# Performance work log

Hardware: AMD Instinct MI355X
Metric: run time of the kernel (lower is better)

## Reference

```python
import jax, jax.numpy as jnp
import numpy as np

D_MODEL = 1024
PATTERNS = 8
BETA = 1.0


def setup_inputs() -> dict:
    key = jax.random.key(0)
    k_h, k_p, k_w, k_b = jax.random.split(key, 4)
    h = jax.random.normal(k_h, (8, 8192, D_MODEL), dtype=jnp.float32)
    patterns = jax.random.normal(k_p, (PATTERNS, D_MODEL), dtype=jnp.float32)
    # nn.Linear(d_model, d_model): weight [out, in], bias [out]
    bound = 1.0 / np.sqrt(D_MODEL)
    proj_w = jax.random.uniform(k_w, (D_MODEL, D_MODEL), minval=-bound, maxval=bound, dtype=jnp.float32)
    proj_b = jax.random.uniform(k_b, (D_MODEL,), minval=-bound, maxval=bound, dtype=jnp.float32)
    return {"h": h, "patterns": patterns, "proj_w": proj_w, "proj_b": proj_b}


def reference(h, patterns, proj_w, proj_b):
    # scores: [B, S, P] = softmax(beta * h @ patterns^T)
    scores = jax.nn.softmax(BETA * jnp.einsum("bsd,pd->bsp", h, patterns), axis=-1)
    # read: [B, S, D]
    read = jnp.einsum("bsp,pd->bsd", scores, patterns)
    # proj(h + read): Linear applies x @ W^T + b
    return jnp.einsum("bsd,ed->bse", h + read, proj_w) + proj_b
```

## Files before the change

### kernel.cpp

```cpp
#include <hip/hip_runtime.h>
#include <hip/hip_bf16.h>
#include <stdint.h>

#define DM 1024
#define NPAT 8
#define NKT 16
#define LDS_A 0
#define LDS_B 65536

typedef __bf16 bf16x8_t __attribute__((ext_vector_type(8)));
typedef float f32x4_t __attribute__((ext_vector_type(4)));
typedef unsigned short u16;

typedef const __attribute__((address_space(1))) void* gas_ptr;
typedef __attribute__((address_space(3))) void* las_ptr;

__device__ __forceinline__ u16 f2bf(float x) {
  uint32_t u = __float_as_uint(x);
  uint32_t r = (u + 0x7FFFu + ((u >> 16) & 1u)) >> 16;
  return (u16)r;
}

__global__ __launch_bounds__(256) void k0_cvt_w(const float* __restrict__ w,
                                                u16* __restrict__ wb) {
  int i = blockIdx.x * 256 + threadIdx.x;
  float4 v = ((const float4*)w)[i];
  ushort4 o;
  o.x = f2bf(v.x); o.y = f2bf(v.y); o.z = f2bf(v.z); o.w = f2bf(v.w);
  ((ushort4*)wb)[i] = o;
}

__global__ __launch_bounds__(256) void k1_hopfield(const float* __restrict__ h,
                                                   const float* __restrict__ pat,
                                                   u16* __restrict__ A, int M) {
  __shared__ float patL[NPAT * DM];
  const int tid = threadIdx.x;
  {
    const float4* p4 = (const float4*)pat;
    float4* l4 = (float4*)patL;
#pragma unroll
    for (int i = 0; i < (NPAT * DM / 4) / 256; ++i)
      l4[i * 256 + tid] = p4[i * 256 + tid];
  }
  __syncthreads();

  const int lane = tid & 63;
  const int wid = (blockIdx.x << 2) | (tid >> 6);
  const int nw = gridDim.x << 2;
  const f32x4_t* h4 = (const f32x4_t*)h;
  const f32x4_t* pl4 = (const f32x4_t*)patL;
  ushort4* A4 = (ushort4*)A;

  for (int rp = wid; rp < (M >> 1); rp += nw) {
    const size_t r0 = (size_t)rp << 1;
    f32x4_t hv0[4], hv1[4];
#pragma unroll
    for (int j = 0; j < 4; ++j) {
      hv0[j] = __builtin_nontemporal_load(&h4[r0 * 256 + j * 64 + lane]);
      hv1[j] = __builtin_nontemporal_load(&h4[(r0 + 1) * 256 + j * 64 + lane]);
    }
    float d0[NPAT], d1[NPAT];
#pragma unroll
    for (int p = 0; p < NPAT; ++p) {
      float a = 0.f, b = 0.f;
#pragma unroll
      for (int j = 0; j < 4; ++j) {
        f32x4_t pv = pl4[p * 256 + j * 64 + lane];
#pragma unroll
        for (int e = 0; e < 4; ++e) {
          a = fmaf(hv0[j][e], pv[e], a);
          b = fmaf(hv1[j][e], pv[e], b);
        }
      }
      d0[p] = a; d1[p] = b;
    }
#pragma unroll
    for (int p = 0; p < NPAT; ++p) {
#pragma unroll
      for (int o = 32; o > 0; o >>= 1) {
        d0[p] += __shfl_xor(d0[p], o);
        d1[p] += __shfl_xor(d1[p], o);
      }
    }
    float m0 = d0[0], m1 = d1[0];
#pragma unroll
    for (int p = 1; p < NPAT; ++p) { m0 = fmaxf(m0, d0[p]); m1 = fmaxf(m1, d1[p]); }
    float s0 = 0.f, s1 = 0.f;
#pragma unroll
    for (int p = 0; p < NPAT; ++p) {
      d0[p] = __expf(d0[p] - m0); s0 += d0[p];
      d1[p] = __expf(d1[p] - m1); s1 += d1[p];
    }
    const float i0 = 1.f / s0, i1 = 1.f / s1;
#pragma unroll
    for (int p = 0; p < NPAT; ++p) { d0[p] *= i0; d1[p] *= i1; }

#pragma unroll
    for (int j = 0; j < 4; ++j) {
      f32x4_t a0 = hv0[j], a1 = hv1[j];
#pragma unroll
      for (int p = 0; p < NPAT; ++p) {
        f32x4_t pv = pl4[p * 256 + j * 64 + lane];
#pragma unroll
        for (int e = 0; e < 4; ++e) {
          a0[e] = fmaf(d0[p], pv[e], a0[e]);
          a1[e] = fmaf(d1[p], pv[e], a1[e]);
        }
      }
      ushort4 o0, o1;
      o0.x = f2bf(a0[0]); o0.y = f2bf(a0[1]); o0.z = f2bf(a0[2]); o0.w = f2bf(a0[3]);
      o1.x = f2bf(a1[0]); o1.y = f2bf(a1[1]); o1.z = f2bf(a1[2]); o1.w = f2bf(a1[3]);
      A4[r0 * 256 + j * 64 + lane] = o0;
      A4[(r0 + 1) * 256 + j * 64 + lane] = o1;
    }
  }
}

#define STAGE(matBase, regionOff, kt, hf, bufOff)                                        \
  do {                                                                                   \
    const u16* _s = (matBase) + (size_t)((hf)*128) * DM + (kt)*64;                       \
    char* _d = lds + (regionOff) + (bufOff) + (hf)*16384;                                \
    __builtin_amdgcn_global_load_lds((gas_ptr)(_s + go0), (las_ptr)(_d + L0), 16, 0, 0); \
    __builtin_amdgcn_global_load_lds((gas_ptr)(_s + go1), (las_ptr)(_d + L1), 16, 0, 0); \
  } while (0)

#define RD(p) (*(const bf16x8_t*)(p))

__global__ __launch_bounds__(512, 2) void k2_gemm(const u16* __restrict__ A,
                                                  const u16* __restrict__ B,
                                                  const float* __restrict__ bias,
                                                  float* __restrict__ C, int M) {
  __shared__ __align__(16) char lds[131072];
  const int tid = threadIdx.x;
  const int lane = tid & 63;
  const int wave = tid >> 6;
  const int wm = wave >> 2;
  const int wn = wave & 3;
  const int r16 = lane & 15, kg = lane >> 4;

  const int bid = blockIdx.x;
  const int swz = (bid & 7) * 128 + (bid >> 3);
  const int tn = swz & 3, tm = swz >> 2;

  const u16* Ab = A + (size_t)tm * 256 * DM;
  const u16* Bb = B + (size_t)tn * 256 * DM;

  const uint32_t L0 = (uint32_t)tid * 16;
  const uint32_t L1 = 8192u + (uint32_t)tid * 16;
  const uint32_t S0 = L0 ^ (((L0 >> 7) & 7u) << 4);
  const uint32_t S1 = L1 ^ (((L1 >> 7) & 7u) << 4);
  const uint32_t go0 = (S0 >> 7) * DM + ((S0 & 127u) >> 1);
  const uint32_t go1 = (S1 >> 7) * DM + ((S1 & 127u) >> 1);

  const uint32_t flip = (uint32_t)(r16 & 7) << 4;
  const uint32_t aoff0 = ((uint32_t)(r16 * 128 + kg * 16)) ^ flip;
  const uint32_t aoff1 = ((uint32_t)(r16 * 128 + 64 + kg * 16)) ^ flip;
  const uint32_t brow = (uint32_t)((wn & 1) * 64 + r16);
  const uint32_t boff0 = ((uint32_t)(brow * 128 + kg * 16)) ^ flip;
  const uint32_t boff1 = ((uint32_t)(brow * 128 + 64 + kg * 16)) ^ flip;
  const uint32_t aHalfSel = (uint32_t)wm * 16384;
  const uint32_t bHalfSel = (uint32_t)(wn >> 1) * 16384;

  f32x4_t acc[8][4] = {};
  bf16x8_t aq[4][2], bl[2][2], bh[2][2];

  STAGE(Bb, LDS_B, 0, 0, 0);
  STAGE(Ab, LDS_A, 0, 0, 0);
  STAGE(Bb, LDS_B, 0, 1, 0);
  STAGE(Ab, LDS_A, 0, 1, 0);
  STAGE(Bb, LDS_B, 1, 0, 32768);
  STAGE(Ab, LDS_A, 1, 0, 32768);
  asm volatile("s_waitcnt vmcnt(4)");
  __builtin_amdgcn_s_barrier();

  for (int t = 0; t < NKT; ++t) {
    const uint32_t co = (uint32_t)(t & 1) << 15;
    const uint32_t no = co ^ 32768u;
    const char* a0 = lds + LDS_A + co + aHalfSel + aoff0;
    const char* a1 = lds + LDS_A + co + aHalfSel + aoff1;
    const char* b0 = lds + LDS_B + co + bHalfSel + boff0;
    const char* b1 = lds + LDS_B + co + bHalfSel + boff1;

#pragma unroll
    for (int m = 0; m < 4; ++m) { aq[m][0] = RD(a0 + m * 2048); aq[m][1] = RD(a1 + m * 2048); }
#pragma unroll
    for (int n = 0; n < 2; ++n) { bl[n][0] = RD(b0 + n * 2048); bl[n][1] = RD(b1 + n * 2048); }
    if (t + 1 < NKT) STAGE(Bb, LDS_B, t + 1, 1, no);
    __builtin_amdgcn_s_barrier();
    asm volatile("s_waitcnt lgkmcnt(0)");
    __builtin_amdgcn_s_setprio(1);
#pragma unroll
    for (int m = 0; m < 4; ++m)
#pragma unroll
      for (int n = 0; n < 2; ++n)
#pragma unroll
        for (int ks = 0; ks < 2; ++ks)
          acc[m][n] = __builtin_amdgcn_mfma_f32_16x16x32_bf16(aq[m][ks], bl[n][ks], acc[m][n], 0, 0, 0);
    __builtin_amdgcn_s_setprio(0);
    __builtin_amdgcn_s_barrier();

#pragma unroll
    for (int n = 0; n < 2; ++n) { bh[n][0] = RD(b0 + (n + 2) * 2048); bh[n][1] = RD(b1 + (n + 2) * 2048); }
    if (t + 1 < NKT) STAGE(Ab, LDS_A, t + 1, 1, no);
    __builtin_amdgcn_s_barrier();
    asm volatile("s_waitcnt lgkmcnt(0)");
    __builtin_amdgcn_s_setprio(1);
#pragma unroll
    for (int m = 0; m < 4; ++m)
#pragma unroll
      for (int n = 0; n < 2; ++n)
#pragma unroll
        for (int ks = 0; ks < 2; ++ks)
          acc[m][n + 2] = __builtin_amdgcn_mfma_f32_16x16x32_bf16(aq[m][ks], bh[n][ks], acc[m][n + 2], 0, 0, 0);
    __builtin_amdgcn_s_setprio(0);
    __builtin_amdgcn_s_barrier();

#pragma unroll
    for (int m = 0; m < 4; ++m) { aq[m][0] = RD(a0 + (m + 4) * 2048); aq[m][1] = RD(a1 + (m + 4) * 2048); }
    if (t + 2 < NKT) STAGE(Bb, LDS_B, t + 2, 0, co);
    __builtin_amdgcn_s_barrier();
    asm volatile("s_waitcnt lgkmcnt(0)");
    __builtin_amdgcn_s_setprio(1);
#pragma unroll
    for (int m = 0; m < 4; ++m)
#pragma unroll
      for (int n = 0; n < 2; ++n)
#pragma unroll
        for (int ks = 0; ks < 2; ++ks)
          acc[m + 4][n] = __builtin_amdgcn_mfma_f32_16x16x32_bf16(aq[m][ks], bl[n][ks], acc[m + 4][n], 0, 0, 0);
    __builtin_amdgcn_s_setprio(0);
    __builtin_amdgcn_s_barrier();

    if (t + 2 < NKT) STAGE(Ab, LDS_A, t + 2, 0, co);
    __builtin_amdgcn_s_barrier();
    __builtin_amdgcn_s_setprio(1);
#pragma unroll
    for (int m = 0; m < 4; ++m)
#pragma unroll
      for (int n = 0; n < 2; ++n)
#pragma unroll
        for (int ks = 0; ks < 2; ++ks)
          acc[m + 4][n + 2] = __builtin_amdgcn_mfma_f32_16x16x32_bf16(aq[m][ks], bh[n][ks], acc[m + 4][n + 2], 0, 0, 0);
    __builtin_amdgcn_s_setprio(0);
    if (t < NKT - 1) {
      if (t + 2 < NKT) asm volatile("s_waitcnt vmcnt(4)");
      else             asm volatile("s_waitcnt vmcnt(0)");
    }
    __builtin_amdgcn_s_barrier();
  }

  const int colB = tn * 256 + wn * 64 + r16;
  const int rowB = tm * 256 + wm * 128 + kg * 4;
  float bvv[4];
#pragma unroll
  for (int n = 0; n < 4; ++n) bvv[n] = bias[colB + n * 16];
#pragma unroll
  for (int m = 0; m < 8; ++m) {
#pragma unroll
    for (int r = 0; r < 4; ++r) {
      float* cp = C + (size_t)(rowB + m * 16 + r) * DM + colB;
#pragma unroll
      for (int n = 0; n < 4; ++n) cp[n * 16] = acc[m][n][r] + bvv[n];
    }
  }
}

extern "C" void kernel_launch(void* const* d_in, const int* in_sizes, int n_in,
                              void* d_out, int out_size, void* d_ws, size_t ws_size,
                              hipStream_t stream) {
  const float* h = (const float*)d_in[0];
  const float* pat = (const float*)d_in[1];
  const float* w = (const float*)d_in[2];
  const float* b = (const float*)d_in[3];
  float* out = (float*)d_out;
  const int M = in_sizes[0] / DM;

  u16* Wb = (u16*)d_ws;
  u16* Abf = (u16*)d_ws + (size_t)DM * DM;

  k0_cvt_w<<<DM * DM / 4 / 256, 256, 0, stream>>>(w, Wb);
  k1_hopfield<<<2048, 256, 0, stream>>>(h, pat, Abf, M);
  k2_gemm<<<(M / 256) * (DM / 256), 512, 0, stream>>>(Abf, Wb, b, out, M);
}
```

Before: 230.2 us.

## Make GEMM blocks loop over all N tiles and overlap epilogue stores with compute

```diff
diff --git a/kernel.cpp b/kernel.cpp
--- a/kernel.cpp
+++ b/kernel.cpp
@@ -4,7 +4,6 @@
 
 #define DM 1024
 #define NPAT 8
-#define NKT 16
 #define LDS_A 0
 #define LDS_B 65536
 
@@ -116,15 +115,23 @@
   }
 }
 
-#define STAGE(matBase, regionOff, kt, hf, bufOff)                                        \
+#define STAGE(basePtr, regionOff, kt, hf, bufOff)                                        \
   do {                                                                                   \
-    const u16* _s = (matBase) + (size_t)((hf)*128) * DM + (kt)*64;                       \
+    const u16* _s = (basePtr) + (size_t)((hf)*128) * DM + (kt)*64;                       \
     char* _d = lds + (regionOff) + (bufOff) + (hf)*16384;                                \
     __builtin_amdgcn_global_load_lds((gas_ptr)(_s + go0), (las_ptr)(_d + L0), 16, 0, 0); \
     __builtin_amdgcn_global_load_lds((gas_ptr)(_s + go1), (las_ptr)(_d + L1), 16, 0, 0); \
   } while (0)
 
 #define RD(p) (*(const bf16x8_t*)(p))
+
+#define STCASE(k)                                                                  \
+  case (k): {                                                                      \
+    _Pragma("unroll") for (int j = 0; j < 8; ++j) {                                \
+      const int mm = (k) >> 1, rr = ((k) & 1) * 2 + (j >> 2), nn = j & 3;          \
+      C[(size_t)(rowB + mm * 16 + rr) * DM + colB2 + nn * 16] = acc2[mm][nn][rr];  \
+    }                                                                              \
+  } break;
 
 __global__ __launch_bounds__(512, 2) void k2_gemm(const u16* __restrict__ A,
                                                   const u16* __restrict__ B,
@@ -138,12 +145,8 @@
   const int wn = wave & 3;
   const int r16 = lane & 15, kg = lane >> 4;
 
-  const int bid = blockIdx.x;
-  const int swz = (bid & 7) * 128 + (bid >> 3);
-  const int tn = swz & 3, tm = swz >> 2;
-
+  const int tm = blockIdx.x;
   const u16* Ab = A + (size_t)tm * 256 * DM;
-  const u16* Bb = B + (size_t)tn * 256 * DM;
 
   const uint32_t L0 = (uint32_t)tid * 16;
   const uint32_t L1 = 8192u + (uint32_t)tid * 16;
@@ -161,20 +164,53 @@
   const uint32_t aHalfSel = (uint32_t)wm * 16384;
   const uint32_t bHalfSel = (uint32_t)(wn >> 1) * 16384;
 
+  const int rowB = tm * 256 + wm * 128 + kg * 4;
+  const int colL = wn * 64 + r16;
+
+  float bvv[4];
+#pragma unroll
+  for (int n = 0; n < 4; ++n) bvv[n] = bias[colL + n * 16];
+
   f32x4_t acc[8][4] = {};
+  f32x4_t acc2[8][4];
   bf16x8_t aq[4][2], bl[2][2], bh[2][2];
 
-  STAGE(Bb, LDS_B, 0, 0, 0);
+  STAGE(B, LDS_B, 0, 0, 0);
   STAGE(Ab, LDS_A, 0, 0, 0);
-  STAGE(Bb, LDS_B, 0, 1, 0);
+  STAGE(B, LDS_B, 0, 1, 0);
   STAGE(Ab, LDS_A, 0, 1, 0);
-  STAGE(Bb, LDS_B, 1, 0, 32768);
+  STAGE(B, LDS_B, 1, 0, 32768);
   STAGE(Ab, LDS_A, 1, 0, 32768);
   asm volatile("s_waitcnt vmcnt(4)");
   __builtin_amdgcn_s_barrier();
 
-  for (int t = 0; t < NKT; ++t) {
-    const uint32_t co = (uint32_t)(t & 1) << 15;
+#pragma unroll 2
+  for (int u = 0; u < 64; ++u) {
+    if ((u & 15) == 0 && u > 0) {
+#pragma unroll
+      for (int m = 0; m < 8; ++m)
+#pragma unroll
+        for (int n = 0; n < 4; ++n)
+#pragma unroll
+          for (int r = 0; r < 4; ++r) {
+            acc2[m][n][r] = acc[m][n][r] + bvv[n];
+            acc[m][n][r] = 0.f;
+          }
+      const int gn = u >> 4;
+#pragma unroll
+      for (int n = 0; n < 4; ++n) bvv[n] = bias[gn * 256 + colL + n * 16];
+    }
+    if (u >= 16) {
+      const int colB2 = ((u >> 4) - 1) * 256 + colL;
+      switch (u & 15) {
+        STCASE(0) STCASE(1) STCASE(2) STCASE(3)
+        STCASE(4) STCASE(5) STCASE(6) STCASE(7)
+        STCASE(8) STCASE(9) STCASE(10) STCASE(11)
+        STCASE(12) STCASE(13) STCASE(14) STCASE(15)
+      }
+    }
+
+    const uint32_t co = (uint32_t)(u & 1) << 15;
     const uint32_t no = co ^ 32768u;
     const char* a0 = lds + LDS_A + co + aHalfSel + aoff0;
     const char* a1 = lds + LDS_A + co + aHalfSel + aoff1;
@@ -185,7 +221,7 @@
     for (int m = 0; m < 4; ++m) { aq[m][0] = RD(a0 + m * 2048); aq[m][1] = RD(a1 + m * 2048); }
 #pragma unroll
     for (int n = 0; n < 2; ++n) { bl[n][0] = RD(b0 + n * 2048); bl[n][1] = RD(b1 + n * 2048); }
-    if (t + 1 < NKT) STAGE(Bb, LDS_B, t + 1, 1, no);
+    if (u + 1 < 64) STAGE(B + (size_t)((u + 1) >> 4) * 256 * DM, LDS_B, (u + 1) & 15, 1, no);
     __builtin_amdgcn_s_barrier();
     asm volatile("s_waitcnt lgkmcnt(0)");
     __builtin_amdgcn_s_setprio(1);
@@ -201,7 +237,7 @@
 
 #pragma unroll
     for (int n = 0; n < 2; ++n) { bh[n][0] = RD(b0 + (n + 2) * 2048); bh[n][1] = RD(b1 + (n + 2) * 2048); }
-    if (t + 1 < NKT) STAGE(Ab, LDS_A, t + 1, 1, no);
+    if (u + 1 < 64) STAGE(Ab, LDS_A, (u + 1) & 15, 1, no);
     __builtin_amdgcn_s_barrier();
     asm volatile("s_waitcnt lgkmcnt(0)");
     __builtin_amdgcn_s_setprio(1);
@@ -217,7 +253,7 @@
 
 #pragma unroll
     for (int m = 0; m < 4; ++m) { aq[m][0] = RD(a0 + (m + 4) * 2048); aq[m][1] = RD(a1 + (m + 4) * 2048); }
-    if (t + 2 < NKT) STAGE(Bb, LDS_B, t + 2, 0, co);
+    if (u + 2 < 64) STAGE(B + (size_t)((u + 2) >> 4) * 256 * DM, LDS_B, (u + 2) & 15, 0, co);
     __builtin_amdgcn_s_barrier();
     asm volatile("s_waitcnt lgkmcnt(0)");
     __builtin_amdgcn_s_setprio(1);
@@ -231,7 +267,7 @@
     __builtin_amdgcn_s_setprio(0);
     __builtin_amdgcn_s_barrier();
 
-    if (t + 2 < NKT) STAGE(Ab, LDS_A, t + 2, 0, co);
+    if (u + 2 < 64) STAGE(Ab, LDS_A, (u + 2) & 15, 0, co);
     __builtin_amdgcn_s_barrier();
     __builtin_amdgcn_s_setprio(1);
 #pragma unroll
@@ -242,18 +278,12 @@
         for (int ks = 0; ks < 2; ++ks)
           acc[m + 4][n + 2] = __builtin_amdgcn_mfma_f32_16x16x32_bf16(aq[m][ks], bh[n][ks], acc[m + 4][n + 2], 0, 0, 0);
     __builtin_amdgcn_s_setprio(0);
-    if (t < NKT - 1) {
-      if (t + 2 < NKT) asm volatile("s_waitcnt vmcnt(4)");
-      else             asm volatile("s_waitcnt vmcnt(0)");
-    }
+    if (u <= 61)      asm volatile("s_waitcnt vmcnt(4)");
+    else if (u == 62) asm volatile("s_waitcnt vmcnt(0)");
     __builtin_amdgcn_s_barrier();
   }
 
-  const int colB = tn * 256 + wn * 64 + r16;
-  const int rowB = tm * 256 + wm * 128 + kg * 4;
-  float bvv[4];
-#pragma unroll
-  for (int n = 0; n < 4; ++n) bvv[n] = bias[colB + n * 16];
+  const int colB = 3 * 256 + colL;
 #pragma unroll
   for (int m = 0; m < 8; ++m) {
 #pragma unroll
@@ -280,5 +310,5 @@
 
   k0_cvt_w<<<DM * DM / 4 / 256, 256, 0, stream>>>(w, Wb);
   k1_hopfield<<<2048, 256, 0, stream>>>(h, pat, Abf, M);
-  k2_gemm<<<(M / 256) * (DM / 256), 512, 0, stream>>>(Abf, Wb, b, out, M);
-}
+  k2_gemm<<<M / 256, 512, 0, stream>>>(Abf, Wb, b, out, M);
+}
```

After: 399.7 us. +73.6%, slower.
